# Kernel optimization log

Hardware: AMD Instinct MI355X
Metric: run time of the kernel (lower is better)

The kernel has to match this reference:

```python
import jax, jax.numpy as jnp
import numpy as np

N_NODES = 50000
EPS_NORM = 1e-12
EPS_ENT = 1e-8

def _l2norm(x):
    # torch.nn.functional.normalize: x / clamp(||x||, min=1e-12)
    n = jnp.sqrt(jnp.sum(x * x, axis=-1, keepdims=True))
    return x / jnp.maximum(n, EPS_NORM)

def _layer(hidden, src, dst, edge_type, multi_emb, proto_emb):
    # hidden: [N,H]; multi_emb: [R,P,H]; proto_emb: [P,H]
    inp_j = hidden[src]                          # [E,H] gather
    rel_basis = multi_emb[edge_type]             # [E,P,H] gather
    sims = jnp.einsum('eh,ph->ep', _l2norm(inp_j), _l2norm(proto_emb))  # cosine sim [E,P]
    proto_proba = jax.nn.softmax(sims, axis=1)   # [E,P]
    msg = jnp.einsum('ep,eph->eh', proto_proba, rel_basis)              # [E,H]
    ent = -jnp.sum(proto_proba * jnp.log(proto_proba + EPS_ENT), axis=1)  # [E]
    logits = -ent
    # scatter_softmax over destination index
    seg_max = jax.ops.segment_max(logits, dst, num_segments=N_NODES)
    ex = jnp.exp(logits - seg_max[dst])
    denom = jax.ops.segment_sum(ex, dst, num_segments=N_NODES)
    attn = ex / denom[dst]                       # [E]
    out = jax.ops.segment_sum(attn[:, None] * msg, dst, num_segments=N_NODES)  # [N,H]
    return out

def setup_inputs() -> dict:
    key = jax.random.key(0)
    ks = jax.random.split(key, 6)
    E = 800000
    H, R, P, L = 128, 18, 18, 3  # num_layers=4 -> 3 NBFCluttr layers
    edge_index = jax.random.randint(ks[0], (2, E), 0, N_NODES, dtype=jnp.int64) if jax.config.read('jax_enable_x64') else jax.random.randint(ks[0], (2, E), 0, N_NODES, dtype=jnp.int32)
    edge_type = jax.random.randint(ks[1], (E,), 0, R, dtype=edge_index.dtype)
    tail_indices = jax.random.randint(ks[2], (1024,), 0, N_NODES, dtype=edge_index.dtype)
    multi_embeddings = jax.random.uniform(ks[3], (L, R, P, H), dtype=jnp.float32)
    proto_embeddings = jax.random.uniform(ks[4], (L, P, H), dtype=jnp.float32)
    source_embedding = jax.random.uniform(ks[5], (H,), dtype=jnp.float32)
    return {"edge_index": edge_index, "edge_type": edge_type, "tail_indices": tail_indices,
            "multi_embeddings": multi_embeddings, "proto_embeddings": proto_embeddings,
            "source_embedding": source_embedding}

def reference(edge_index, edge_type, tail_indices, multi_embeddings, proto_embeddings, source_embedding):
    src, dst = edge_index[0], edge_index[1]
    H = source_embedding.shape[0]
    # boundary condition: source node gets source_embedding, rest zero
    hidden = jnp.zeros((N_NODES, H), dtype=source_embedding.dtype).at[0].set(source_embedding)
    L = multi_embeddings.shape[0]
    for l in range(L):  # small fixed loop over structurally distinct layers
        hidden = _layer(hidden, src, dst, edge_type, multi_embeddings[l], proto_embeddings[l])
    # apply_classifier, eval_mode=True, use_mlp_classifier=False -> cosine sims to last layer prototypes
    out_emb = hidden[tail_indices]               # [B,H]
    sims = jnp.einsum('nh,ph->np', _l2norm(out_emb), _l2norm(proto_embeddings[-1]))
    return sims  # gumbel_softmax_sample with eval_mode=True returns logits unchanged
```

## Files before the change

kernel.cpp:

```cpp
#include <hip/hip_runtime.h>
#include <hip/hip_bf16.h>


#define N_NODES 50000
#define H 128
#define P 18
#define RP 324
#define KPAD 352
#define K0PAD 32
#define ELLW 64
#define NPART 8
#define NODES_PER_PART 6250
#define PREP_MAIN_BLOCKS 384
#define N0CAP 1024

typedef _Float16 half8 __attribute__((ext_vector_type(8)));
typedef _Float16 half2v __attribute__((ext_vector_type(2)));
typedef float floatx4 __attribute__((ext_vector_type(4)));

__global__ __launch_bounds__(256) void ell_kernel(const int* __restrict__ src,
                                                  const int* __restrict__ dst,
                                                  const int* __restrict__ etype,
                                                  unsigned* __restrict__ cur,
                                                  unsigned* __restrict__ ep,
                                                  unsigned* __restrict__ n0list, int E) {
  int part = blockIdx.x & (NPART - 1);
  int i = (blockIdx.x >> 3) * 256 + threadIdx.x;
  if (i >= E) return;
  int d = dst[i];
  int lo = part * NODES_PER_PART;
  if (d < lo || d >= lo + NODES_PER_PART) return;
  int s = src[i];
  int r = etype[i];
  unsigned pos = atomicAdd(&cur[d], 1u);
  if (pos < ELLW)
    ep[(size_t)d * ELLW + pos] = (unsigned)s | ((unsigned)r << 20);
  if (s == 0) {
    unsigned ix = atomicAdd(&cur[N_NODES], 1u);
    if (ix < N0CAP) n0list[ix] = (unsigned)d | ((unsigned)r << 20);
  }
}

__global__ __launch_bounds__(256) void prep_kernel(const float* __restrict__ multi,
                                                   const float* __restrict__ proto,
                                                   const float* __restrict__ semb,
                                                   float* __restrict__ pN,
                                                   _Float16* __restrict__ Btg,
                                                   _Float16* __restrict__ Btl0,
                                                   _Float16* __restrict__ BtD,
                                                   unsigned* __restrict__ cur) {
  int bid = blockIdx.x;
  if (bid >= PREP_MAIN_BLOCKS) {
    int wave = threadIdx.x >> 6, l = threadIdx.x & 63;
    int row = (bid - PREP_MAIN_BLOCKS) * 4 + wave;
    if (row >= 54) return;
    float a = proto[row * H + l], b = proto[row * H + 64 + l];
    float ss = a * a + b * b;
    for (int m = 32; m > 0; m >>= 1) ss += __shfl_xor(ss, m, 64);
    float inv = 1.f / fmaxf(sqrtf(ss), 1e-12f);
    pN[row * H + l] = a * inv;
    pN[row * H + 64 + l] = b * inv;
    return;
  }
  int idx = bid * 256 + threadIdx.x;
  if (idx <= N_NODES) cur[idx] = 0u;
  if (idx < 2 * H * KPAD) {
    int l = idx / (H * KPAD), rem = idx - l * (H * KPAD);
    int h = rem / KPAD, k = rem - h * KPAD;
    const float* B = multi + (size_t)(l + 1) * RP * H;
    Btg[idx] = (k < RP) ? (_Float16)B[k * H + h] : (_Float16)0.f;
    return;
  }
  int idx2 = idx - 2 * H * KPAD;
  if (idx2 >= H * 64) return;
  int h = idx2 >> 6, k = idx2 & 63;
  float s0 = semb[k], s1 = semb[k + 64];
  float ssq = s0 * s0 + s1 * s1;
  float dq[P];
#pragma unroll
  for (int p = 0; p < P; p++) {
    float a = proto[p * H + k], b = proto[p * H + 64 + k];
    float rn = a * a + b * b;
    for (int m = 32; m > 0; m >>= 1) rn += __shfl_xor(rn, m, 64);
    float rinv = 1.f / fmaxf(sqrtf(rn), 1e-12f);
    dq[p] = (s0 * a + s1 * b) * rinv;
  }
  for (int m = 1; m <= 32; m <<= 1) {
    ssq += __shfl_xor(ssq, m, 64);
#pragma unroll
    for (int p = 0; p < P; p++) dq[p] += __shfl_xor(dq[p], m, 64);
  }
  float inv = 1.f / fmaxf(sqrtf(ssq), 1e-12f);
  float sum = 0.f;
#pragma unroll
  for (int p = 0; p < P; p++) {
    dq[p] = __expf(dq[p] * inv - 1.f);
    sum += dq[p];
  }
  float isum = 1.f / sum, ent = 0.f;
#pragma unroll
  for (int p = 0; p < P; p++) {
    dq[p] *= isum;
    ent -= dq[p] * __logf(dq[p] + 1e-8f);
  }
  float w = __expf(-ent);
  float pr = 1.f / 18.f, ent0 = 0.f;
#pragma unroll
  for (int p = 0; p < P; p++) ent0 -= pr * __logf(pr + 1e-8f);
  float qc = __expf(-ent0) * pr;
  if (k < K0PAD) {
    float v = 0.f;
    if (k < P) {
#pragma unroll
      for (int p = 0; p < P; p++) v += qc * multi[(k * P + p) * H + h];
    }
    Btl0[h * K0PAD + k] = (_Float16)v;
  } else if (k < K0PAD + P) {
    int r = k - K0PAD;
    float v = 0.f;
#pragma unroll
    for (int p = 0; p < P; p++) v += (w * dq[p] - qc) * multi[(r * P + p) * H + h];
    BtD[r * H + h] = (_Float16)v;
  }
}

__global__ __launch_bounds__(256) void hist_kernel(const unsigned* __restrict__ ep,
                                                   const unsigned* __restrict__ cur,
                                                   _Float16* __restrict__ M, int n) {
  int wave = threadIdx.x >> 6, lane = threadIdx.x & 63;
  int nd = blockIdx.x * 4 + wave;
  if (nd >= n) return;
  int cnt = (int)cur[nd];
  if (cnt > ELLW) cnt = ELLW;
  bool a = lane < cnt;
  unsigned pk = a ? ep[(size_t)nd * ELLW + lane] : 0xFFFFFFFFu;
  int r = (int)(pk >> 20);
  float creg = 0.f;
#pragma unroll
  for (int rr = 0; rr < P; rr++) {
    unsigned long long m = __ballot(a && (r == rr));
    if (lane == rr) creg = (float)__popcll(m);
  }
  if (lane < K0PAD) M[(size_t)nd * K0PAD + lane] = (_Float16)creg;
}

__global__ __launch_bounds__(256) void patch_kernel(const unsigned* __restrict__ cur,
                                                    const unsigned* __restrict__ n0list,
                                                    const _Float16* __restrict__ M,
                                                    const _Float16* __restrict__ Btl0,
                                                    const _Float16* __restrict__ BtD,
                                                    const float* __restrict__ pN,
                                                    _Float16* __restrict__ q) {
  int n0 = (int)cur[N_NODES];
  if (n0 > N0CAP) n0 = N0CAP;
  int wave = threadIdx.x >> 6, lane = threadIdx.x & 63;
  int e = blockIdx.x * 4 + wave;
  if (e >= n0) return;
  unsigned pe = n0list[e];
  int d = (int)(pe & 0xFFFFFu);
  for (int e2 = 0; e2 < e; e2++)
    if ((int)(n0list[e2] & 0xFFFFFu) == d) return;
  float ya = 0.f, yb = 0.f;
#pragma unroll
  for (int r = 0; r < P; r++) {
    float c = (float)M[(size_t)d * K0PAD + r];
    ya += c * (float)Btl0[lane * K0PAD + r];
    yb += c * (float)Btl0[(lane + 64) * K0PAD + r];
  }
  for (int e2 = e; e2 < n0; e2++) {
    unsigned p2 = n0list[e2];
    if ((int)(p2 & 0xFFFFFu) != d) continue;
    int r2 = (int)(p2 >> 20);
    ya += (float)BtD[r2 * H + lane];
    yb += (float)BtD[r2 * H + lane + 64];
  }
  float ss = ya * ya + yb * yb;
  float dot[P];
#pragma unroll
  for (int p = 0; p < P; p++) dot[p] = ya * pN[p * H + lane] + yb * pN[p * H + lane + 64];
  for (int m = 1; m <= 32; m <<= 1) {
    ss += __shfl_xor(ss, m, 64);
#pragma unroll
    for (int p = 0; p < P; p++) dot[p] += __shfl_xor(dot[p], m, 64);
  }
  float inv = 1.f / fmaxf(sqrtf(ss), 1e-12f);
  float sum = 0.f;
#pragma unroll
  for (int p = 0; p < P; p++) {
    dot[p] = __expf(dot[p] * inv - 1.f);
    sum += dot[p];
  }
  float isum = 1.f / sum, ent = 0.f;
#pragma unroll
  for (int p = 0; p < P; p++) {
    dot[p] *= isum;
    ent -= dot[p] * __logf(dot[p] + 1e-8f);
  }
  float w = __expf(-ent);
  if (lane < P) q[(size_t)d * P + lane] = (_Float16)(w * dot[lane]);
}

__global__ __launch_bounds__(256) void scatter_kernel(const unsigned* __restrict__ ep,
                                                      const unsigned* __restrict__ cur,
                                                      const _Float16* __restrict__ q,
                                                      const int* __restrict__ tl,
                                                      _Float16* __restrict__ M, int n) {
  __shared__ float sl[4][3 * RP];
  int wave = threadIdx.x >> 6, lane = threadIdx.x & 63;
  int t = blockIdx.x * 4 + wave;
  float* s0 = sl[wave];
  for (int i = lane; i < 3 * RP; i += 64) s0[i] = 0.f;
  int sub = lane / 18;
  int j = lane - sub * 18;
  bool act = (sub < 3) && (t < n);
  int cnt = 0;
  size_t b = 0;
  if (t < n) {
    int nd = tl ? tl[t] : t;
    b = (size_t)nd * ELLW;
    cnt = (int)cur[nd];
    if (cnt > ELLW) cnt = ELLW;
  }
  float* ms = s0 + (sub < 3 ? sub : 0) * RP;
  for (int it = 0; it < cnt; it += 18) {
    bool aa[6];
    unsigned pk[6];
    float qv[6];
#pragma unroll
    for (int u = 0; u < 6; u++) {
      int e = it + 3 * u + sub;
      aa[u] = act && (e < cnt);
      pk[u] = aa[u] ? ep[b + e] : 0u;
    }
#pragma unroll
    for (int u = 0; u < 6; u++)
      qv[u] = aa[u] ? (float)q[(size_t)(pk[u] & 0xFFFFFu) * P + j] : 0.f;
#pragma unroll
    for (int u = 0; u < 6; u++)
      if (aa[u]) ms[(pk[u] >> 20) * P + j] += qv[u];
  }
  if (t < n) {
    for (int wd = lane; wd < RP / 2; wd += 64) {
      float2 x0 = *(const float2*)(s0 + 2 * wd);
      float2 x1 = *(const float2*)(s0 + RP + 2 * wd);
      float2 x2 = *(const float2*)(s0 + 2 * RP + 2 * wd);
      half2v hv;
      hv[0] = (_Float16)(x0.x + x1.x + x2.x);
      hv[1] = (_Float16)(x0.y + x1.y + x2.y);
      *(half2v*)(M + (size_t)t * KPAD + 2 * wd) = hv;
    }
    for (int wd = RP / 2 + lane; wd < KPAD / 2; wd += 64) {
      half2v z = {};
      *(half2v*)(M + (size_t)t * KPAD + 2 * wd) = z;
    }
  }
}

template <int MODE>
__global__ __launch_bounds__(256) void gemm_kernel(const _Float16* __restrict__ M,
                                                   const _Float16* __restrict__ Bt,
                                                   const float* __restrict__ pN,
                                                   void* __restrict__ out_ptr, int n,
                                                   int kpad) {
  __shared__ float smem_f[64 * 132];
  _Float16* As = (_Float16*)smem_f;
  _Float16* Bs = (_Float16*)(smem_f + 1024);
  int tid = threadIdx.x;
  int wave = tid >> 6, lane = tid & 63;
  int m15 = lane & 15, quad = lane >> 4;
  int n0 = blockIdx.x * 64;
  floatx4 acc[4][2] = {};

  __shared__ float pns[4 * P * 36];
  for (int i = tid; i < 4 * P * 32; i += 256) {
    int s = i / (P * 32), r = i - s * (P * 32);
    int p = r >> 5, kk = r & 31;
    pns[s * (P * 36) + p * 36 + kk] = pN[p * H + s * 32 + kk];
  }

  for (int kt = 0; kt < (kpad >> 5); kt++) {
    int k0 = kt * 32;
    __syncthreads();
    {
      int row = tid >> 2, kc = (tid & 3) * 8;
      int gr = n0 + row;
      half8 v = {};
      if (gr < n) v = *(const half8*)(M + (size_t)gr * kpad + k0 + kc);
      *(half8*)(As + row * 32 + kc) = v;
    }
    {
      int col = tid >> 1, kc = (tid & 1) * 16;
      const _Float16* srcp = Bt + (size_t)col * kpad + k0 + kc;
      *(half8*)(Bs + col * 32 + kc) = *(const half8*)srcp;
      *(half8*)(Bs + col * 32 + kc + 8) = *(const half8*)(srcp + 8);
    }
    __syncthreads();
    half8 bfrag0 = *(const half8*)(Bs + (wave * 32 + m15) * 32 + quad * 8);
    half8 bfrag1 = *(const half8*)(Bs + (wave * 32 + 16 + m15) * 32 + quad * 8);
#pragma unroll
    for (int mt = 0; mt < 4; mt++) {
      half8 afrag = *(const half8*)(As + (mt * 16 + m15) * 32 + quad * 8);
      acc[mt][0] = __builtin_amdgcn_mfma_f32_16x16x32_f16(afrag, bfrag0, acc[mt][0], 0, 0, 0);
      acc[mt][1] = __builtin_amdgcn_mfma_f32_16x16x32_f16(afrag, bfrag1, acc[mt][1], 0, 0, 0);
    }
  }
  __syncthreads();
#pragma unroll
  for (int mt = 0; mt < 4; mt++)
#pragma unroll
    for (int c = 0; c < 2; c++)
#pragma unroll
      for (int reg = 0; reg < 4; reg++)
        smem_f[(mt * 16 + quad * 4 + reg) * 132 + wave * 32 + c * 16 + m15] = acc[mt][c][reg];
  __syncthreads();
  int node = tid >> 2, sub = tid & 3;
  int gnode = n0 + node;
  const float* trow = smem_f + node * 132 + sub * 32;
  const float* ps = pns + sub * (P * 36);
  float ss = 0.f;
  float dot[P];
#pragma unroll
  for (int p = 0; p < P; p++) dot[p] = 0.f;
#pragma unroll
  for (int k4 = 0; k4 < 8; k4++) {
    float4 y = *(const float4*)(trow + k4 * 4);
    ss += y.x * y.x + y.y * y.y + y.z * y.z + y.w * y.w;
#pragma unroll
    for (int p = 0; p < P; p++) {
      float4 b = *(const float4*)(ps + p * 36 + k4 * 4);
      dot[p] += y.x * b.x + y.y * b.y + y.z * b.z + y.w * b.w;
    }
  }
  for (int m = 1; m <= 2; m <<= 1) {
    ss += __shfl_xor(ss, m, 64);
#pragma unroll
    for (int p = 0; p < P; p++) dot[p] += __shfl_xor(dot[p], m, 64);
  }
  if (gnode < n) {
    float inv = 1.f / fmaxf(sqrtf(ss), 1e-12f);
    if (MODE == 1) {
      float* outp = (float*)out_ptr;
      for (int p = sub; p < P; p += 4) outp[(size_t)gnode * P + p] = dot[p] * inv;
    } else {
      float sum = 0.f;
#pragma unroll
      for (int p = 0; p < P; p++) {
        dot[p] = __expf(dot[p] * inv - 1.f);
        sum += dot[p];
      }
      float isum = 1.f / sum, ent = 0.f;
#pragma unroll
      for (int p = 0; p < P; p++) {
        dot[p] *= isum;
        ent -= dot[p] * __logf(dot[p] + 1e-8f);
      }
      float w = __expf(-ent);
      _Float16* qp = (_Float16*)out_ptr;
      for (int p = sub; p < P; p += 4) qp[(size_t)gnode * P + p] = (_Float16)(w * dot[p]);
    }
  }
}

extern "C" void kernel_launch(void* const* d_in, const int* in_sizes, int n_in,
                              void* d_out, int out_size, void* d_ws, size_t ws_size,
                              hipStream_t stream) {
  const int* eidx = (const int*)d_in[0];
  int E = in_sizes[0] / 2;
  const int* src = eidx;
  const int* dst = eidx + E;
  const int* etype = (const int*)d_in[1];
  const int* tails = (const int*)d_in[2];
  int T = in_sizes[2];
  const float* multi = (const float*)d_in[3];
  const float* proto = (const float*)d_in[4];
  const float* semb = (const float*)d_in[5];
  float* out = (float*)d_out;

  char* w = (char*)d_ws;
  auto alloc = [&](size_t bytes) {
    char* p = w;
    w += (bytes + 255) & ~(size_t)255;
    return p;
  };
  _Float16* q = (_Float16*)alloc((size_t)N_NODES * P * 2);
  float* pNs = (float*)alloc((size_t)3 * P * H * 4);
  _Float16* Mg = (_Float16*)alloc((size_t)N_NODES * KPAD * 2);
  _Float16* Btg = (_Float16*)alloc((size_t)2 * H * KPAD * 2);
  _Float16* Btl0 = (_Float16*)alloc((size_t)H * K0PAD * 2);
  _Float16* BtD = (_Float16*)alloc((size_t)P * H * 2);
  unsigned* cur = (unsigned*)alloc((size_t)(N_NODES + 1) * 4);
  unsigned* n0list = (unsigned*)alloc((size_t)N0CAP * 4);
  unsigned* ep = (unsigned*)alloc((size_t)N_NODES * ELLW * 4);

  int eb = (E + 255) / 256;

  prep_kernel<<<PREP_MAIN_BLOCKS + 14, 256, 0, stream>>>(multi, proto, semb, pNs, Btg,
                                                         Btl0, BtD, cur);

  ell_kernel<<<eb * NPART, 256, 0, stream>>>(src, dst, etype, cur, ep, n0list, E);

  hist_kernel<<<(N_NODES + 3) / 4, 256, 0, stream>>>(ep, cur, Mg, N_NODES);
  gemm_kernel<0><<<(N_NODES + 63) / 64, 256, 0, stream>>>(Mg, Btl0, pNs + (size_t)1 * P * H, q,
                                                          N_NODES, K0PAD);
  patch_kernel<<<(N0CAP + 3) / 4, 256, 0, stream>>>(cur, n0list, Mg, Btl0, BtD,
                                                    pNs + (size_t)1 * P * H, q);

  scatter_kernel<<<(N_NODES + 3) / 4, 256, 0, stream>>>(ep, cur, q, nullptr, Mg, N_NODES);
  gemm_kernel<0><<<(N_NODES + 63) / 64, 256, 0, stream>>>(Mg, Btg, pNs + (size_t)2 * P * H, q,
                                                          N_NODES, KPAD);

  scatter_kernel<<<(T + 3) / 4, 256, 0, stream>>>(ep, cur, q, tails, Mg, T);
  gemm_kernel<1><<<(T + 63) / 64, 256, 0, stream>>>(Mg, Btg + (size_t)H * KPAD,
                                                    pNs + (size_t)2 * P * H, out, T, KPAD);
}
```

Measured before the change: 232.6 us.

## Fold layer-1 GEMM into histogram via precomputed Gram and prototype-dot tables

Precomputes small 18x18 tables in the prep kernel: dot products of per-relation layer-0 messages with normalized prototypes, and the Gram matrix of those messages. The histogram kernel then computes each node's cosine similarities, norm, softmax and entropy-weighted q straight from its relation counts. This removes the layer-1 GEMM launch and the fp16 count-matrix round trip. The patch kernel now recomputes counts from the ELL lists, since the count matrix is no longer written. It adds extra prep blocks and a small per-wave reduction.

```diff
diff --git a/kernel.cpp b/kernel.cpp
--- a/kernel.cpp
+++ b/kernel.cpp
@@ -12,6 +12,8 @@
 #define NPART 8
 #define NODES_PER_PART 6250
 #define PREP_MAIN_BLOCKS 384
+#define PREP_PN_BLOCKS 14
+#define PREP_GS_BLOCKS 162
 #define N0CAP 1024
 
 typedef _Float16 half8 __attribute__((ext_vector_type(8)));
@@ -48,8 +50,50 @@
                                                    _Float16* __restrict__ Btg,
                                                    _Float16* __restrict__ Btl0,
                                                    _Float16* __restrict__ BtD,
+                                                   float* __restrict__ GS,
                                                    unsigned* __restrict__ cur) {
   int bid = blockIdx.x;
+  if (bid >= PREP_MAIN_BLOCKS + PREP_PN_BLOCKS) {
+    int wave = threadIdx.x >> 6, lane = threadIdx.x & 63;
+    int pi = (bid - PREP_MAIN_BLOCKS - PREP_PN_BLOCKS) * 4 + wave;
+    if (pi >= 648) return;
+    float pr = 1.f / 18.f, ent0 = 0.f;
+#pragma unroll
+    for (int p = 0; p < P; p++) ent0 -= pr * __logf(pr + 1e-8f);
+    float qc = __expf(-ent0) * pr;
+    bool isG = pi < 324;
+    int rr = isG ? pi / P : (pi - 324) / P;
+    int cc = isG ? pi - rr * P : (pi - 324) - rr * P;
+    float ca = 0.f, cb = 0.f;
+#pragma unroll
+    for (int q2 = 0; q2 < P; q2++) {
+      ca += multi[(rr * P + q2) * H + lane];
+      cb += multi[(rr * P + q2) * H + lane + 64];
+    }
+    ca *= qc; cb *= qc;
+    float xa, xb, rn = 0.f;
+    if (isG) {
+      xa = proto[(P + cc) * H + lane];
+      xb = proto[(P + cc) * H + lane + 64];
+      rn = xa * xa + xb * xb;
+    } else {
+      xa = 0.f; xb = 0.f;
+#pragma unroll
+      for (int q2 = 0; q2 < P; q2++) {
+        xa += multi[(cc * P + q2) * H + lane];
+        xb += multi[(cc * P + q2) * H + lane + 64];
+      }
+      xa *= qc; xb *= qc;
+    }
+    float dotp = ca * xa + cb * xb;
+    for (int m = 32; m > 0; m >>= 1) {
+      dotp += __shfl_xor(dotp, m, 64);
+      rn += __shfl_xor(rn, m, 64);
+    }
+    float val = isG ? dotp / fmaxf(sqrtf(rn), 1e-12f) : dotp;
+    if (lane == 0) GS[pi] = val;
+    return;
+  }
   if (bid >= PREP_MAIN_BLOCKS) {
     int wave = threadIdx.x >> 6, l = threadIdx.x & 63;
     int row = (bid - PREP_MAIN_BLOCKS) * 4 + wave;
@@ -124,9 +168,13 @@
   }
 }
 
-__global__ __launch_bounds__(256) void hist_kernel(const unsigned* __restrict__ ep,
-                                                   const unsigned* __restrict__ cur,
-                                                   _Float16* __restrict__ M, int n) {
+__global__ __launch_bounds__(256) void histq_kernel(const unsigned* __restrict__ ep,
+                                                    const unsigned* __restrict__ cur,
+                                                    const float* __restrict__ GS,
+                                                    _Float16* __restrict__ q, int n) {
+  __shared__ float gs[648];
+  for (int i = threadIdx.x; i < 648; i += 256) gs[i] = GS[i];
+  __syncthreads();
   int wave = threadIdx.x >> 6, lane = threadIdx.x & 63;
   int nd = blockIdx.x * 4 + wave;
   if (nd >= n) return;
@@ -141,12 +189,33 @@
     unsigned long long m = __ballot(a && (r == rr));
     if (lane == rr) creg = (float)__popcll(m);
   }
-  if (lane < K0PAD) M[(size_t)nd * K0PAD + lane] = (_Float16)creg;
+  float dot = 0.f, t = 0.f;
+#pragma unroll
+  for (int rr = 0; rr < P; rr++) {
+    float c = __shfl(creg, rr, 64);
+    if (lane < P) {
+      dot += c * gs[rr * P + lane];
+      t += c * gs[324 + rr * P + lane];
+    }
+  }
+  float u = (lane < P) ? creg * t : 0.f;
+  for (int m = 1; m <= 16; m <<= 1) u += __shfl_xor(u, m, 32);
+  float ss = u;
+  float inv = 1.f / fmaxf(sqrtf(ss), 1e-12f);
+  float e = (lane < P) ? __expf(dot * inv - 1.f) : 0.f;
+  float sum = e;
+  for (int m = 1; m <= 16; m <<= 1) sum += __shfl_xor(sum, m, 32);
+  float prb = e / sum;
+  float term = (lane < P) ? prb * __logf(prb + 1e-8f) : 0.f;
+  float ent = term;
+  for (int m = 1; m <= 16; m <<= 1) ent += __shfl_xor(ent, m, 32);
+  float w = __expf(ent);
+  if (lane < P) q[(size_t)nd * P + lane] = (_Float16)(w * prb);
 }
 
 __global__ __launch_bounds__(256) void patch_kernel(const unsigned* __restrict__ cur,
                                                     const unsigned* __restrict__ n0list,
-                                                    const _Float16* __restrict__ M,
+                                                    const unsigned* __restrict__ ep,
                                                     const _Float16* __restrict__ Btl0,
                                                     const _Float16* __restrict__ BtD,
                                                     const float* __restrict__ pN,
@@ -160,12 +229,23 @@
   int d = (int)(pe & 0xFFFFFu);
   for (int e2 = 0; e2 < e; e2++)
     if ((int)(n0list[e2] & 0xFFFFFu) == d) return;
+  int cnt = (int)cur[d];
+  if (cnt > ELLW) cnt = ELLW;
+  bool a = lane < cnt;
+  unsigned pk2 = a ? ep[(size_t)d * ELLW + lane] : 0xFFFFFFFFu;
+  int rr0 = (int)(pk2 >> 20);
+  float creg = 0.f;
+#pragma unroll
+  for (int rr = 0; rr < P; rr++) {
+    unsigned long long m = __ballot(a && (rr0 == rr));
+    if (lane == rr) creg = (float)__popcll(m);
+  }
   float ya = 0.f, yb = 0.f;
 #pragma unroll
-  for (int r = 0; r < P; r++) {
-    float c = (float)M[(size_t)d * K0PAD + r];
-    ya += c * (float)Btl0[lane * K0PAD + r];
-    yb += c * (float)Btl0[(lane + 64) * K0PAD + r];
+  for (int rr = 0; rr < P; rr++) {
+    float c = __shfl(creg, rr, 64);
+    ya += c * (float)Btl0[lane * K0PAD + rr];
+    yb += c * (float)Btl0[(lane + 64) * K0PAD + rr];
   }
   for (int e2 = e; e2 < n0; e2++) {
     unsigned p2 = n0list[e2];
@@ -384,6 +464,7 @@
   };
   _Float16* q = (_Float16*)alloc((size_t)N_NODES * P * 2);
   float* pNs = (float*)alloc((size_t)3 * P * H * 4);
+  float* GS = (float*)alloc((size_t)648 * 4);
   _Float16* Mg = (_Float16*)alloc((size_t)N_NODES * KPAD * 2);
   _Float16* Btg = (_Float16*)alloc((size_t)2 * H * KPAD * 2);
   _Float16* Btl0 = (_Float16*)alloc((size_t)H * K0PAD * 2);
@@ -394,15 +475,13 @@
 
   int eb = (E + 255) / 256;
 
-  prep_kernel<<<PREP_MAIN_BLOCKS + 14, 256, 0, stream>>>(multi, proto, semb, pNs, Btg,
-                                                         Btl0, BtD, cur);
+  prep_kernel<<<PREP_MAIN_BLOCKS + PREP_PN_BLOCKS + PREP_GS_BLOCKS, 256, 0, stream>>>(
+      multi, proto, semb, pNs, Btg, Btl0, BtD, GS, cur);
 
   ell_kernel<<<eb * NPART, 256, 0, stream>>>(src, dst, etype, cur, ep, n0list, E);
 
-  hist_kernel<<<(N_NODES + 3) / 4, 256, 0, stream>>>(ep, cur, Mg, N_NODES);
-  gemm_kernel<0><<<(N_NODES + 63) / 64, 256, 0, stream>>>(Mg, Btl0, pNs + (size_t)1 * P * H, q,
-                                                          N_NODES, K0PAD);
-  patch_kernel<<<(N0CAP + 3) / 4, 256, 0, stream>>>(cur, n0list, Mg, Btl0, BtD,
+  histq_kernel<<<(N_NODES + 3) / 4, 256, 0, stream>>>(ep, cur, GS, q, N_NODES);
+  patch_kernel<<<(N0CAP + 3) / 4, 256, 0, stream>>>(cur, n0list, ep, Btl0, BtD,
                                                     pNs + (size_t)1 * P * H, q);
 
   scatter_kernel<<<(N_NODES + 3) / 4, 256, 0, stream>>>(ep, cur, q, nullptr, Mg, N_NODES);
```

After: 230.9 us. Within noise of the previous version (-0.7%).
